# Optimization experiments

Hardware: AMD Instinct MI355X
Metric: run time of the kernel (lower is better)

## Reference

```python
import jax, jax.numpy as jnp
import numpy as np

# Fixed-shape (jit-compatible) isosurface extraction. The original module calls
# mcubes.marching_cubes on CPU, which has data-dependent output shapes. Here we
# implement the same math (zero-isosurface of -level with linear edge
# interpolation, vertices returned in normalized [0,1]^3 coords with axes
# swapped [2,1,0]) via a marching-tetrahedra decomposition with PADDED outputs:
# a dense vertex buffer (one slot per tet-edge) plus triangle indices and a
# validity mask instead of stream compaction.

RES = 64

# cube corner numbering (offsets in array-index space)
CUBE_OFF = np.array([[0,0,0],[1,0,0],[1,1,0],[0,1,0],
                     [0,0,1],[1,0,1],[1,1,1],[0,1,1]], dtype=np.int32)
# 6-tetrahedra split of the cube around diagonal 0-6
TETS = np.array([[0,5,1,6],[0,1,2,6],[0,2,3,6],
                 [0,3,7,6],[0,7,4,6],[0,4,5,6]], dtype=np.int32)
# tet edges (pairs of tet-local vertex ids)
EDGES = np.array([[0,1],[1,2],[2,0],[0,3],[1,3],[2,3]], dtype=np.int32)

# marching-tetrahedra triangle table: case -> up to 2 triangles of edge ids
_CASES = {1:[[0,3,2]], 2:[[0,1,4]], 3:[[2,3,4],[2,4,1]], 4:[[1,5,2]],
          5:[[0,1,5],[0,5,3]], 6:[[0,4,5],[0,5,2]], 7:[[3,4,5]], 8:[[3,5,4]],
          9:[[0,2,5],[0,5,4]], 10:[[0,3,5],[0,5,1]], 11:[[1,2,5]],
          12:[[1,4,3],[1,3,2]], 13:[[0,4,1]], 14:[[0,2,3]]}
TET_TRIS = np.full((16,2,3), -1, dtype=np.int32)
for c, tris in _CASES.items():
    for i, tr in enumerate(tris):
        TET_TRIS[c, i] = tr


def setup_inputs() -> dict:
    key = jax.random.key(0)
    level = jax.random.normal(key, (RES**3,), dtype=jnp.float32)
    return {"level": level}


def reference(level):
    R = RES
    f = -level.reshape(R, R, R)  # original negates before extraction
    C = (R - 1) ** 3
    # corner scalar values per cell: [C, 8]
    cf = jnp.stack([f[o[0]:o[0]+R-1, o[1]:o[1]+R-1, o[2]:o[2]+R-1].reshape(-1)
                    for o in CUBE_OFF], axis=-1)
    # corner positions per cell in array-index space: [C, 8, 3]
    ax = jnp.arange(R - 1)
    base = jnp.stack(jnp.meshgrid(ax, ax, ax, indexing='ij'), -1).reshape(-1, 1, 3)
    cp = (base + CUBE_OFF[None]).astype(f.dtype)
    # gather per-tet values/positions: [C,6,4], [C,6,4,3]
    fv = cf[:, TETS]
    pv = cp[:, TETS]
    # classification: 4-bit case per tet, bit set where value > 0
    case = ((fv > 0).astype(jnp.int32) * np.array([1, 2, 4, 8], dtype=np.int32)).sum(-1)  # [C,6]
    # linear interpolation on every tet edge (padded; unused slots are garbage)
    fa = fv[..., EDGES[:, 0]]; fb = fv[..., EDGES[:, 1]]          # [C,6,6]
    pa = pv[:, :, EDGES[:, 0]]; pb = pv[:, :, EDGES[:, 1]]        # [C,6,6,3]
    d = fa - fb
    d_safe = jnp.where(jnp.abs(d) < 1e-8, 1e-8, d)
    t = jnp.clip(fa / d_safe, 0.0, 1.0)
    v = pa + t[..., None] * (pb - pa)                              # [C,6,6,3]
    # swap axes (a0,a1,a2)->(a2,a1,a0) and normalize to [0,1], as in original
    v_pos = v.reshape(-1, 3)[:, ::-1] / (R - 1.0)                  # [C*36, 3]
    # triangle emission via table lookup, padded to 2 tris/tet
    te = TET_TRIS[case]                                            # [C,6,2,3]
    valid = te[..., 0] >= 0                                        # [C,6,2]
    base_e = (jnp.arange(C * 6, dtype=jnp.int32) * 6).reshape(C, 6, 1, 1)
    tri = base_e + jnp.maximum(te, 0)                              # [C,6,2,3]
    return v_pos, tri.reshape(-1, 3), valid.reshape(-1)
```

## Files before the change

kernel.cpp:

```cpp
#include <hip/hip_runtime.h>

#define RES       64
#define CM1       63
#define NCELL     250047
#define NTET      1500282
#define V_ELEMS   27005076
#define TRI_ELEMS 9001692

#define TPB 256

__constant__ int c_TETS[6][4] = {
    {0,5,1,6},{0,1,2,6},{0,2,3,6},{0,3,7,6},{0,7,4,6},{0,4,5,6}
};
__constant__ int c_OFF[8][3] = {
    {0,0,0},{1,0,0},{1,1,0},{0,1,0},{0,0,1},{1,0,1},{1,1,1},{0,1,1}
};
__constant__ int c_TRI[16][6] = {
    {-1,-1,-1,-1,-1,-1},
    { 0, 3, 2,-1,-1,-1},
    { 0, 1, 4,-1,-1,-1},
    { 2, 3, 4, 2, 4, 1},
    { 1, 5, 2,-1,-1,-1},
    { 0, 1, 5, 0, 5, 3},
    { 0, 4, 5, 0, 5, 2},
    { 3, 4, 5,-1,-1,-1},
    { 3, 5, 4,-1,-1,-1},
    { 0, 2, 5, 0, 5, 4},
    { 0, 3, 5, 0, 5, 1},
    { 1, 2, 5,-1,-1,-1},
    { 1, 4, 3, 1, 3, 2},
    { 0, 4, 1,-1,-1,-1},
    { 0, 2, 3,-1,-1,-1},
    {-1,-1,-1,-1,-1,-1}
};

__global__ __launch_bounds__(TPB) void mc_kernel(const float* __restrict__ level,
                                                 float* __restrict__ out)
{
    __shared__ float sv[TPB * 18];
    __shared__ float st[TPB * 6];
    __shared__ float sl[TPB * 2];

    int t  = threadIdx.x;
    int w  = t >> 6;
    int l  = t & 63;
    int g0 = blockIdx.x * TPB;
    int g  = g0 + t;
    int ntet = NTET - g0; if (ntet > TPB) ntet = TPB;
    int ntw = ntet - w * 64;
    ntw = ntw < 0 ? 0 : (ntw > 64 ? 64 : ntw);

    if (l < ntw) {
        int cell = g / 6;
        int tet  = g - cell * 6;
        int i    = cell / (CM1 * CM1);
        int rem  = cell - i * (CM1 * CM1);
        int j    = rem / CM1;
        int k    = rem - j * CM1;
        int base = i * (RES * RES) + j * RES + k;

        float fv[4], px[4], py[4], pz[4];
        #pragma unroll
        for (int vi = 0; vi < 4; ++vi) {
            int c  = c_TETS[tet][vi];
            int ox = c_OFF[c][0], oy = c_OFF[c][1], oz = c_OFF[c][2];
            fv[vi] = -level[base + ox * (RES * RES) + oy * RES + oz];
            px[vi] = (float)(i + ox);
            py[vi] = (float)(j + oy);
            pz[vi] = (float)(k + oz);
        }

        int cs = (fv[0] > 0.0f ? 1 : 0) | (fv[1] > 0.0f ? 2 : 0)
               | (fv[2] > 0.0f ? 4 : 0) | (fv[3] > 0.0f ? 8 : 0);

        const int EA[6] = {0, 1, 2, 0, 1, 2};
        const int EB[6] = {1, 2, 0, 3, 3, 3};

        const float inv63 = 1.0f / 63.0f;
        #pragma unroll
        for (int e = 0; e < 6; ++e) {
            int a = EA[e], b = EB[e];
            float fa = fv[a], fb = fv[b];
            float d  = fa - fb;
            float ds = (fabsf(d) < 1e-8f) ? 1e-8f : d;
            float tt = fa * __builtin_amdgcn_rcpf(ds);
            tt = fminf(fmaxf(tt, 0.0f), 1.0f);
            float vx = px[a] + tt * (px[b] - px[a]);
            float vy = py[a] + tt * (py[b] - py[a]);
            float vz = pz[a] + tt * (pz[b] - pz[a]);
            sv[t * 18 + e * 3 + 0] = vz * inv63;
            sv[t * 18 + e * 3 + 1] = vy * inv63;
            sv[t * 18 + e * 3 + 2] = vx * inv63;
        }

        int base6 = g * 6;
        #pragma unroll
        for (int tr = 0; tr < 2; ++tr) {
            int t0 = c_TRI[cs][tr * 3 + 0];
            int t1 = c_TRI[cs][tr * 3 + 1];
            int t2 = c_TRI[cs][tr * 3 + 2];
            sl[t * 2 + tr] = (t0 >= 0) ? 1.0f : 0.0f;
            int m0 = t0 > 0 ? t0 : 0;
            int m1 = t1 > 0 ? t1 : 0;
            int m2 = t2 > 0 ? t2 : 0;
            st[t * 6 + tr * 3 + 0] = (float)(base6 + m0);
            st[t * 6 + tr * 3 + 1] = (float)(base6 + m1);
            st[t * 6 + tr * 3 + 2] = (float)(base6 + m2);
        }
    }

    __builtin_amdgcn_wave_barrier();

    if (ntw == 64) {
        float4*       gv = (float4*)(out + (size_t)g0 * 18) + (size_t)w * 288;
        const float4* lv = (const float4*)sv + w * 288;
        #pragma unroll
        for (int n = 0; n < 4; ++n) gv[l + n * 64] = lv[l + n * 64];
        if (l < 32) gv[l + 256] = lv[l + 256];

        float4*       gt = (float4*)(out + V_ELEMS + (size_t)g0 * 6) + (size_t)w * 96;
        const float4* lt = (const float4*)st + w * 96;
        gt[l] = lt[l];
        if (l < 32) gt[l + 64] = lt[l + 64];

        float4*       gl = (float4*)(out + V_ELEMS + TRI_ELEMS + (size_t)g0 * 2) + (size_t)w * 32;
        const float4* ll = (const float4*)sl + w * 32;
        if (l < 32) gl[l] = ll[l];
    } else if (ntw > 0) {
        int n4v = (ntw * 18) >> 2;
        float4*       gv = (float4*)(out + (size_t)g0 * 18) + (size_t)w * 288;
        const float4* lv = (const float4*)sv + w * 288;
        for (int idx = l; idx < n4v; idx += 64) gv[idx] = lv[idx];

        int n4t = (ntw * 6) >> 2;
        float4*       gt = (float4*)(out + V_ELEMS + (size_t)g0 * 6) + (size_t)w * 96;
        const float4* lt = (const float4*)st + w * 96;
        for (int idx = l; idx < n4t; idx += 64) gt[idx] = lt[idx];

        int n4l = (ntw * 2) >> 2;
        float4*       gl = (float4*)(out + V_ELEMS + TRI_ELEMS + (size_t)g0 * 2) + (size_t)w * 32;
        const float4* ll = (const float4*)sl + w * 32;
        for (int idx = l; idx < n4l; idx += 64) gl[idx] = ll[idx];
    }
}

extern "C" void kernel_launch(void* const* d_in, const int* in_sizes, int n_in,
                              void* d_out, int out_size, void* d_ws, size_t ws_size,
                              hipStream_t stream) {
    const float* level = (const float*)d_in[0];
    float* out = (float*)d_out;
    int blocks = (NTET + TPB - 1) / TPB;
    mc_kernel<<<blocks, TPB, 0, stream>>>(level, out);
}
```

Before: 30.92 us.

## Split kernel into separate block groups per output stream

Partitions the grid into three block ranges: one writes vertex positions, one writes triangle indices (1024 tets per block), and one writes validity masks (1024 tets per block). Each block group then writes a single contiguous output region, which is meant to improve write streaming and give each block a smaller shared-memory footprint. In exchange, the tet case classification and its four level loads are recomputed in both the triangle and mask block groups. The vertex blocks no longer load anything beyond the level values they already needed.

```diff
diff --git a/kernel.cpp b/kernel.cpp
--- a/kernel.cpp
+++ b/kernel.cpp
@@ -8,6 +8,8 @@
 #define TRI_ELEMS 9001692
 
 #define TPB 256
+#define NA  5861
+#define NBC 1466
 
 __constant__ int c_TETS[6][4] = {
     {0,5,1,6},{0,1,2,6},{0,2,3,6},{0,3,7,6},{0,7,4,6},{0,4,5,6}
@@ -16,131 +18,156 @@
     {0,0,0},{1,0,0},{1,1,0},{0,1,0},{0,0,1},{1,0,1},{1,1,1},{0,1,1}
 };
 __constant__ int c_TRI[16][6] = {
-    {-1,-1,-1,-1,-1,-1},
-    { 0, 3, 2,-1,-1,-1},
-    { 0, 1, 4,-1,-1,-1},
-    { 2, 3, 4, 2, 4, 1},
-    { 1, 5, 2,-1,-1,-1},
-    { 0, 1, 5, 0, 5, 3},
-    { 0, 4, 5, 0, 5, 2},
-    { 3, 4, 5,-1,-1,-1},
-    { 3, 5, 4,-1,-1,-1},
-    { 0, 2, 5, 0, 5, 4},
-    { 0, 3, 5, 0, 5, 1},
-    { 1, 2, 5,-1,-1,-1},
-    { 1, 4, 3, 1, 3, 2},
-    { 0, 4, 1,-1,-1,-1},
-    { 0, 2, 3,-1,-1,-1},
-    {-1,-1,-1,-1,-1,-1}
+    {-1,-1,-1,-1,-1,-1},{ 0, 3, 2,-1,-1,-1},{ 0, 1, 4,-1,-1,-1},{ 2, 3, 4, 2, 4, 1},
+    { 1, 5, 2,-1,-1,-1},{ 0, 1, 5, 0, 5, 3},{ 0, 4, 5, 0, 5, 2},{ 3, 4, 5,-1,-1,-1},
+    { 3, 5, 4,-1,-1,-1},{ 0, 2, 5, 0, 5, 4},{ 0, 3, 5, 0, 5, 1},{ 1, 2, 5,-1,-1,-1},
+    { 1, 4, 3, 1, 3, 2},{ 0, 4, 1,-1,-1,-1},{ 0, 2, 3,-1,-1,-1},{-1,-1,-1,-1,-1,-1}
 };
+
+__device__ __forceinline__ void decode(int g, int& i, int& j, int& k, int& tet, int& base) {
+    int cell = g / 6;
+    tet  = g - cell * 6;
+    i    = cell / (CM1 * CM1);
+    int rem = cell - i * (CM1 * CM1);
+    j    = rem / CM1;
+    k    = rem - j * CM1;
+    base = i * (RES * RES) + j * RES + k;
+}
+
+__device__ __forceinline__ int tet_case(const float* __restrict__ level, int g) {
+    int i, j, k, tet, base;
+    decode(g, i, j, k, tet, base);
+    int cs = 0;
+    #pragma unroll
+    for (int vi = 0; vi < 4; ++vi) {
+        int c  = c_TETS[tet][vi];
+        float f = -level[base + c_OFF[c][0] * (RES * RES) + c_OFF[c][1] * RES + c_OFF[c][2]];
+        cs |= (f > 0.0f) ? (1 << vi) : 0;
+    }
+    return cs;
+}
 
 __global__ __launch_bounds__(TPB) void mc_kernel(const float* __restrict__ level,
                                                  float* __restrict__ out)
 {
-    __shared__ float sv[TPB * 18];
-    __shared__ float st[TPB * 6];
-    __shared__ float sl[TPB * 2];
+    __shared__ float s[6144];
 
-    int t  = threadIdx.x;
-    int w  = t >> 6;
-    int l  = t & 63;
-    int g0 = blockIdx.x * TPB;
-    int g  = g0 + t;
-    int ntet = NTET - g0; if (ntet > TPB) ntet = TPB;
-    int ntw = ntet - w * 64;
-    ntw = ntw < 0 ? 0 : (ntw > 64 ? 64 : ntw);
+    int bid = blockIdx.x;
+    int t   = threadIdx.x;
+    int w   = t >> 6;
+    int l   = t & 63;
 
-    if (l < ntw) {
-        int cell = g / 6;
-        int tet  = g - cell * 6;
-        int i    = cell / (CM1 * CM1);
-        int rem  = cell - i * (CM1 * CM1);
-        int j    = rem / CM1;
-        int k    = rem - j * CM1;
-        int base = i * (RES * RES) + j * RES + k;
+    if (bid < NA) {
+        int g0 = bid * TPB;
+        int g  = g0 + t;
+        int ntet = NTET - g0; if (ntet > TPB) ntet = TPB;
+        int ntw  = ntet - w * 64; ntw = ntw < 0 ? 0 : (ntw > 64 ? 64 : ntw);
 
-        float fv[4], px[4], py[4], pz[4];
-        #pragma unroll
-        for (int vi = 0; vi < 4; ++vi) {
-            int c  = c_TETS[tet][vi];
-            int ox = c_OFF[c][0], oy = c_OFF[c][1], oz = c_OFF[c][2];
-            fv[vi] = -level[base + ox * (RES * RES) + oy * RES + oz];
-            px[vi] = (float)(i + ox);
-            py[vi] = (float)(j + oy);
-            pz[vi] = (float)(k + oz);
+        if (l < ntw) {
+            int i, j, k, tet, base;
+            decode(g, i, j, k, tet, base);
+            float fv[4], px[4], py[4], pz[4];
+            #pragma unroll
+            for (int vi = 0; vi < 4; ++vi) {
+                int c  = c_TETS[tet][vi];
+                int ox = c_OFF[c][0], oy = c_OFF[c][1], oz = c_OFF[c][2];
+                fv[vi] = -level[base + ox * (RES * RES) + oy * RES + oz];
+                px[vi] = (float)(i + ox);
+                py[vi] = (float)(j + oy);
+                pz[vi] = (float)(k + oz);
+            }
+            const int EA[6] = {0, 1, 2, 0, 1, 2};
+            const int EB[6] = {1, 2, 0, 3, 3, 3};
+            const float inv63 = 1.0f / 63.0f;
+            #pragma unroll
+            for (int e = 0; e < 6; ++e) {
+                int a = EA[e], b = EB[e];
+                float fa = fv[a], fb = fv[b];
+                float d  = fa - fb;
+                float ds = (fabsf(d) < 1e-8f) ? 1e-8f : d;
+                float tt = fa * __builtin_amdgcn_rcpf(ds);
+                tt = fminf(fmaxf(tt, 0.0f), 1.0f);
+                float vx = px[a] + tt * (px[b] - px[a]);
+                float vy = py[a] + tt * (py[b] - py[a]);
+                float vz = pz[a] + tt * (pz[b] - pz[a]);
+                s[t * 18 + e * 3 + 0] = vz * inv63;
+                s[t * 18 + e * 3 + 1] = vy * inv63;
+                s[t * 18 + e * 3 + 2] = vx * inv63;
+            }
+        }
+        __builtin_amdgcn_wave_barrier();
+
+        float4*       gv = (float4*)(out + (size_t)g0 * 18) + (size_t)w * 288;
+        const float4* lv = (const float4*)s + w * 288;
+        if (ntw == 64) {
+            #pragma unroll
+            for (int n = 0; n < 4; ++n) gv[l + n * 64] = lv[l + n * 64];
+            if (l < 32) gv[l + 256] = lv[l + 256];
+        } else if (ntw > 0) {
+            int n4 = (ntw * 18) >> 2;
+            for (int idx = l; idx < n4; idx += 64) gv[idx] = lv[idx];
         }
 
-        int cs = (fv[0] > 0.0f ? 1 : 0) | (fv[1] > 0.0f ? 2 : 0)
-               | (fv[2] > 0.0f ? 4 : 0) | (fv[3] > 0.0f ? 8 : 0);
+    } else if (bid < NA + NBC) {
+        int bb    = bid - NA;
+        int G0    = bb * 1024;
+        int wbase = G0 + w * 256;
+        int ntw   = NTET - wbase; ntw = ntw < 0 ? 0 : (ntw > 256 ? 256 : ntw);
 
-        const int EA[6] = {0, 1, 2, 0, 1, 2};
-        const int EB[6] = {1, 2, 0, 3, 3, 3};
+        #pragma unroll
+        for (int tt = 0; tt < 4; ++tt) {
+            int idx = tt * 64 + l;
+            if (idx < ntw) {
+                int g  = wbase + idx;
+                int cs = tet_case(level, g);
+                int base6 = g * 6;
+                float* sp = &s[w * 1536 + idx * 6];
+                #pragma unroll
+                for (int n = 0; n < 6; ++n) {
+                    int e = c_TRI[cs][n];
+                    sp[n] = (float)(base6 + (e > 0 ? e : 0));
+                }
+            }
+        }
+        __builtin_amdgcn_wave_barrier();
 
-        const float inv63 = 1.0f / 63.0f;
-        #pragma unroll
-        for (int e = 0; e < 6; ++e) {
-            int a = EA[e], b = EB[e];
-            float fa = fv[a], fb = fv[b];
-            float d  = fa - fb;
-            float ds = (fabsf(d) < 1e-8f) ? 1e-8f : d;
-            float tt = fa * __builtin_amdgcn_rcpf(ds);
-            tt = fminf(fmaxf(tt, 0.0f), 1.0f);
-            float vx = px[a] + tt * (px[b] - px[a]);
-            float vy = py[a] + tt * (py[b] - py[a]);
-            float vz = pz[a] + tt * (pz[b] - pz[a]);
-            sv[t * 18 + e * 3 + 0] = vz * inv63;
-            sv[t * 18 + e * 3 + 1] = vy * inv63;
-            sv[t * 18 + e * 3 + 2] = vx * inv63;
+        float4*       gt = (float4*)(out + V_ELEMS + (size_t)wbase * 6);
+        const float4* lt = (const float4*)s + w * 384;
+        if (ntw == 256) {
+            #pragma unroll
+            for (int p = 0; p < 6; ++p) gt[l + p * 64] = lt[l + p * 64];
+        } else if (ntw > 0) {
+            int n4 = (ntw * 6) >> 2;
+            for (int idx = l; idx < n4; idx += 64) gt[idx] = lt[idx];
         }
 
-        int base6 = g * 6;
+    } else {
+        int cc    = bid - NA - NBC;
+        int G0    = cc * 1024;
+        int wbase = G0 + w * 256;
+        int ntw   = NTET - wbase; ntw = ntw < 0 ? 0 : (ntw > 256 ? 256 : ntw);
+
         #pragma unroll
-        for (int tr = 0; tr < 2; ++tr) {
-            int t0 = c_TRI[cs][tr * 3 + 0];
-            int t1 = c_TRI[cs][tr * 3 + 1];
-            int t2 = c_TRI[cs][tr * 3 + 2];
-            sl[t * 2 + tr] = (t0 >= 0) ? 1.0f : 0.0f;
-            int m0 = t0 > 0 ? t0 : 0;
-            int m1 = t1 > 0 ? t1 : 0;
-            int m2 = t2 > 0 ? t2 : 0;
-            st[t * 6 + tr * 3 + 0] = (float)(base6 + m0);
-            st[t * 6 + tr * 3 + 1] = (float)(base6 + m1);
-            st[t * 6 + tr * 3 + 2] = (float)(base6 + m2);
+        for (int tt = 0; tt < 4; ++tt) {
+            int idx = tt * 64 + l;
+            if (idx < ntw) {
+                int g  = wbase + idx;
+                int cs = tet_case(level, g);
+                s[w * 512 + idx * 2 + 0] = (c_TRI[cs][0] >= 0) ? 1.0f : 0.0f;
+                s[w * 512 + idx * 2 + 1] = (c_TRI[cs][3] >= 0) ? 1.0f : 0.0f;
+            }
         }
-    }
+        __builtin_amdgcn_wave_barrier();
 
-    __builtin_amdgcn_wave_barrier();
-
-    if (ntw == 64) {
-        float4*       gv = (float4*)(out + (size_t)g0 * 18) + (size_t)w * 288;
-        const float4* lv = (const float4*)sv + w * 288;
-        #pragma unroll
-        for (int n = 0; n < 4; ++n) gv[l + n * 64] = lv[l + n * 64];
-        if (l < 32) gv[l + 256] = lv[l + 256];
-
-        float4*       gt = (float4*)(out + V_ELEMS + (size_t)g0 * 6) + (size_t)w * 96;
-        const float4* lt = (const float4*)st + w * 96;
-        gt[l] = lt[l];
-        if (l < 32) gt[l + 64] = lt[l + 64];
-
-        float4*       gl = (float4*)(out + V_ELEMS + TRI_ELEMS + (size_t)g0 * 2) + (size_t)w * 32;
-        const float4* ll = (const float4*)sl + w * 32;
-        if (l < 32) gl[l] = ll[l];
-    } else if (ntw > 0) {
-        int n4v = (ntw * 18) >> 2;
-        float4*       gv = (float4*)(out + (size_t)g0 * 18) + (size_t)w * 288;
-        const float4* lv = (const float4*)sv + w * 288;
-        for (int idx = l; idx < n4v; idx += 64) gv[idx] = lv[idx];
-
-        int n4t = (ntw * 6) >> 2;
-        float4*       gt = (float4*)(out + V_ELEMS + (size_t)g0 * 6) + (size_t)w * 96;
-        const float4* lt = (const float4*)st + w * 96;
-        for (int idx = l; idx < n4t; idx += 64) gt[idx] = lt[idx];
-
-        int n4l = (ntw * 2) >> 2;
-        float4*       gl = (float4*)(out + V_ELEMS + TRI_ELEMS + (size_t)g0 * 2) + (size_t)w * 32;
-        const float4* ll = (const float4*)sl + w * 32;
-        for (int idx = l; idx < n4l; idx += 64) gl[idx] = ll[idx];
+        float4*       gl = (float4*)(out + V_ELEMS + TRI_ELEMS + (size_t)wbase * 2);
+        const float4* ll = (const float4*)s + w * 128;
+        if (ntw == 256) {
+            gl[l]      = ll[l];
+            gl[l + 64] = ll[l + 64];
+        } else if (ntw > 0) {
+            int n4 = (ntw * 2) >> 2;
+            for (int idx = l; idx < n4; idx += 64) gl[idx] = ll[idx];
+        }
     }
 }
 
@@ -149,6 +176,5 @@
                               hipStream_t stream) {
     const float* level = (const float*)d_in[0];
     float* out = (float*)d_out;
-    int blocks = (NTET + TPB - 1) / TPB;
-    mc_kernel<<<blocks, TPB, 0, stream>>>(level, out);
+    mc_kernel<<<NA + 2 * NBC, TPB, 0, stream>>>(level, out);
 }
```

Measured after the change: 41.15 us. 33.1% more time.
